# Optimization experiments

Measured on AMD Instinct MI355X. Metric: run time of the kernel, lower is better.

Reference implementation:

```python
import jax, jax.numpy as jnp
import numpy as np

N_NODES = 100000
N_EDGES = 3200000


def _gcn_conv(x, src, dst, W, b, n_nodes):
    # PyG GCNConv: out = D^{-1/2} (A + I) D^{-1/2} X W + b
    h = x @ W  # [N, out]
    # degree of (A + I) counted at targets (symmetric graph assumption as in PyG norm)
    deg = jax.ops.segment_sum(jnp.ones_like(dst, dtype=h.dtype), dst, num_segments=n_nodes)
    dinv = jnp.where(deg > 0, jax.lax.rsqrt(deg), 0.0)
    norm = dinv[src] * dinv[dst]  # [E_total]
    msg = h[src] * norm[:, None]  # gather + normalize  [E_total, out]
    out = jax.ops.segment_sum(msg, dst, num_segments=n_nodes)  # scatter-add
    return out + b


def setup_inputs() -> dict:
    key = jax.random.key(0)
    k1, k2, k3, k4 = jax.random.split(key, 4)
    x = jax.random.normal(k1, (N_NODES, 1), dtype=jnp.float32)
    edge_index = jax.random.randint(k2, (2, N_EDGES), 0, N_NODES, dtype=jnp.int64)
    W1 = jax.random.normal(k3, (1, 64), dtype=jnp.float32) * (1.0 / np.sqrt(1.0))
    b1 = jnp.zeros((64,), dtype=jnp.float32)
    W2 = jax.random.normal(k4, (64, 2), dtype=jnp.float32) * (1.0 / np.sqrt(64.0))
    b2 = jnp.zeros((2,), dtype=jnp.float32)
    return {"x": x, "edge_index": edge_index, "W1": W1, "b1": b1, "W2": W2, "b2": b2}


def reference(x, edge_index, W1, b1, W2, b2):
    n = x.shape[0]
    # add self-loops as GCNConv does by default
    loops = jnp.arange(n, dtype=edge_index.dtype)
    src = jnp.concatenate([edge_index[0], loops])
    dst = jnp.concatenate([edge_index[1], loops])
    h = _gcn_conv(x, src, dst, W1, b1, n)
    h = jax.nn.relu(h)
    h = _gcn_conv(h, src, dst, W2, b2, n)
    h = jax.nn.log_softmax(h, axis=1)
    out = jnp.mean(h, axis=0)
    return out[None, :]  # [1, 2]
```

## Files before the change

### kernel.cpp

```cpp
#include <hip/hip_runtime.h>


#define TPB 512
#define SORT_BLK 256
#define BSHIFT 7
#define BNODES 128
#define MAXBUCK 1024
#define BSTRIDE 6144


__global__ __launch_bounds__(TPB) void k_sort(const int* __restrict__ ei, int E, int epb,
                                              int nbuck, int* __restrict__ gcur,
                                              unsigned* __restrict__ packed) {
    __shared__ int h[MAXBUCK];
    for (int b = threadIdx.x; b < nbuck; b += TPB) h[b] = 0;
    __syncthreads();
    const int4* d4 = (const int4*)(ei + E);
    int nq = epb >> 2;
    int q0 = blockIdx.x * nq;
    for (int j = threadIdx.x; j < nq; j += TPB) {
        int q = q0 + j;
        int e = q << 2;
        if (e + 3 < E) {
            int4 v = d4[q];
            atomicAdd(&h[v.x >> BSHIFT], 1);
            atomicAdd(&h[v.y >> BSHIFT], 1);
            atomicAdd(&h[v.z >> BSHIFT], 1);
            atomicAdd(&h[v.w >> BSHIFT], 1);
        } else {
            for (int k = 0; k < 4; ++k)
                if (e + k < E) atomicAdd(&h[(ei + E)[e + k] >> BSHIFT], 1);
        }
    }
    __syncthreads();
    for (int b = threadIdx.x; b < nbuck; b += TPB) {
        int c = h[b];
        h[b] = c ? atomicAdd(&gcur[b], c) : 0;
    }
    __syncthreads();
    const int4* s4 = (const int4*)ei;
    for (int j = threadIdx.x; j < nq; j += TPB) {
        int q = q0 + j;
        int e = q << 2;
        if (e + 3 < E) {
            int4 vs = s4[q];
            int4 vd = d4[q];
            int b, p;
            b = vd.x >> BSHIFT; p = atomicAdd(&h[b], 1);
            packed[b * BSTRIDE + p] = ((unsigned)(vd.x & (BNODES - 1)) << 17) | (unsigned)vs.x;
            b = vd.y >> BSHIFT; p = atomicAdd(&h[b], 1);
            packed[b * BSTRIDE + p] = ((unsigned)(vd.y & (BNODES - 1)) << 17) | (unsigned)vs.y;
            b = vd.z >> BSHIFT; p = atomicAdd(&h[b], 1);
            packed[b * BSTRIDE + p] = ((unsigned)(vd.z & (BNODES - 1)) << 17) | (unsigned)vs.z;
            b = vd.w >> BSHIFT; p = atomicAdd(&h[b], 1);
            packed[b * BSTRIDE + p] = ((unsigned)(vd.w & (BNODES - 1)) << 17) | (unsigned)vs.w;
        } else {
            for (int k = 0; k < 4; ++k) {
                int ee = e + k;
                if (ee < E) {
                    int s = ei[ee], d = ei[E + ee];
                    int b = d >> BSHIFT;
                    int p = atomicAdd(&h[b], 1);
                    packed[b * BSTRIDE + p] = ((unsigned)(d & (BNODES - 1)) << 17) | (unsigned)s;
                }
            }
        }
    }
}


__global__ __launch_bounds__(TPB) void k_csr(unsigned* __restrict__ packed,
                                             const int* __restrict__ gcur,
                                             const float* __restrict__ x,
                                             float* __restrict__ dinv,
                                             float* __restrict__ u,
                                             int* __restrict__ rptr, int N) {
    __shared__ int cnt[8][BNODES];
    __shared__ int eptr[BNODES];
    __shared__ unsigned stage[BSTRIDE];
    for (int k = threadIdx.x; k < 8 * BNODES; k += TPB) ((int*)cnt)[k] = 0;
    __syncthreads();
    int b = blockIdx.x;
    int sz = gcur[b];
    unsigned* base = packed + (size_t)b * BSTRIDE;
    const uint4* base4 = (const uint4*)base;
    int wv = threadIdx.x >> 6;
    int nq4 = sz >> 2;
    int half = nq4 >> 1;
    for (int j = threadIdx.x; j < half; j += TPB) {
        uint4 p = base4[j];
        uint4 q = base4[j + half];
        atomicAdd(&cnt[wv][(p.x >> 17) & 127], 1);
        atomicAdd(&cnt[wv][(p.y >> 17) & 127], 1);
        atomicAdd(&cnt[wv][(p.z >> 17) & 127], 1);
        atomicAdd(&cnt[wv][(p.w >> 17) & 127], 1);
        atomicAdd(&cnt[wv][(q.x >> 17) & 127], 1);
        atomicAdd(&cnt[wv][(q.y >> 17) & 127], 1);
        atomicAdd(&cnt[wv][(q.z >> 17) & 127], 1);
        atomicAdd(&cnt[wv][(q.w >> 17) & 127], 1);
    }
    for (int j = half * 8 + threadIdx.x; j < sz; j += TPB) {
        unsigned p = base[j];
        atomicAdd(&cnt[wv][(p >> 17) & 127], 1);
    }
    __syncthreads();
    int tot = 0;
    if (threadIdx.x < BNODES) {
        #pragma unroll
        for (int c = 0; c < 8; ++c) tot += cnt[c][threadIdx.x];
        eptr[threadIdx.x] = tot;
    }
    __syncthreads();
    for (int d = 1; d < BNODES; d <<= 1) {
        int add = 0;
        if (threadIdx.x < BNODES && threadIdx.x >= d) add = eptr[threadIdx.x - d];
        __syncthreads();
        if (threadIdx.x < BNODES) eptr[threadIdx.x] += add;
        __syncthreads();
    }
    if (threadIdx.x < BNODES) {
        int t = threadIdx.x;
        int ex = eptr[t] - tot;
        int run = ex;
        #pragma unroll
        for (int c = 0; c < 8; ++c) { int v = cnt[c][t]; cnt[c][t] = run; run += v; }
        rptr[b * BNODES + t] = ex;
        int node = (b << BSHIFT) + t;
        if (node < N) {
            float di = rsqrtf((float)(tot + 1));
            dinv[node] = di;
            u[node] = di * x[node];
        }
    }
    __syncthreads();
    for (int j = threadIdx.x; j < half; j += TPB) {
        uint4 p = base4[j];
        uint4 q = base4[j + half];
        int pos;
        pos = atomicAdd(&cnt[wv][(p.x >> 17) & 127], 1); stage[pos] = p.x & 0x1FFFF;
        pos = atomicAdd(&cnt[wv][(p.y >> 17) & 127], 1); stage[pos] = p.y & 0x1FFFF;
        pos = atomicAdd(&cnt[wv][(p.z >> 17) & 127], 1); stage[pos] = p.z & 0x1FFFF;
        pos = atomicAdd(&cnt[wv][(p.w >> 17) & 127], 1); stage[pos] = p.w & 0x1FFFF;
        pos = atomicAdd(&cnt[wv][(q.x >> 17) & 127], 1); stage[pos] = q.x & 0x1FFFF;
        pos = atomicAdd(&cnt[wv][(q.y >> 17) & 127], 1); stage[pos] = q.y & 0x1FFFF;
        pos = atomicAdd(&cnt[wv][(q.z >> 17) & 127], 1); stage[pos] = q.z & 0x1FFFF;
        pos = atomicAdd(&cnt[wv][(q.w >> 17) & 127], 1); stage[pos] = q.w & 0x1FFFF;
    }
    for (int j = half * 8 + threadIdx.x; j < sz; j += TPB) {
        unsigned p = base[j];
        int pos = atomicAdd(&cnt[wv][(p >> 17) & 127], 1);
        stage[pos] = p & 0x1FFFF;
    }
    __syncthreads();
    for (int k = threadIdx.x; k < sz; k += TPB) base[k] = stage[k];
}


__global__ __launch_bounds__(TPB) void k_agg1(const unsigned* __restrict__ sorted,
                                              const int* __restrict__ gcur,
                                              const int* __restrict__ rptr,
                                              const float* __restrict__ dinv,
                                              const float* __restrict__ u,
                                              const float* __restrict__ W1,
                                              const float* __restrict__ b1,
                                              const float* __restrict__ W2,
                                              float2* __restrict__ w, int N) {
    __shared__ float sW1[64], sb1[64], sW2[128];
    __shared__ int sptr[BNODES + 1];
    int b = blockIdx.x;
    if (threadIdx.x < 64) { sW1[threadIdx.x] = W1[threadIdx.x]; sb1[threadIdx.x] = b1[threadIdx.x]; }
    else if (threadIdx.x < 192) sW2[threadIdx.x - 64] = W2[threadIdx.x - 64];
    if (threadIdx.x < BNODES) sptr[threadIdx.x] = rptr[b * BNODES + threadIdx.x];
    if (threadIdx.x == 0) sptr[BNODES] = gcur[b];
    __syncthreads();
    int t = threadIdx.x >> 2, k = threadIdx.x & 3;
    const unsigned* base = sorted + (size_t)b * BSTRIDE;
    int s0 = sptr[t], s1 = sptr[t + 1];
    float s = 0.f;
    for (int j = s0 + k; j < s1; j += 4) s += u[base[j] & 0x1FFFF];
    s += __shfl_xor(s, 1, 64);
    s += __shfl_xor(s, 2, 64);
    int node = (b << BSHIFT) + t;
    if (k == 0 && node < N) {
        float di = dinv[node];
        float sv = di * (s + u[node]);
        float z0 = 0.f, z1 = 0.f;
        #pragma unroll
        for (int j = 0; j < 64; ++j) {
            float h = fmaxf(fmaf(sv, sW1[j], sb1[j]), 0.f);
            z0 = fmaf(h, sW2[2 * j], z0);
            z1 = fmaf(h, sW2[2 * j + 1], z1);
        }
        w[node] = make_float2(di * z0, di * z1);
    }
}


__global__ __launch_bounds__(TPB) void k_agg2(const unsigned* __restrict__ sorted,
                                              const int* __restrict__ gcur,
                                              const int* __restrict__ rptr,
                                              const float* __restrict__ dinv,
                                              const float2* __restrict__ w,
                                              const float* __restrict__ b2,
                                              float* __restrict__ accum, int N) {
    __shared__ int sptr[BNODES + 1];
    int b = blockIdx.x;
    if (threadIdx.x < BNODES) sptr[threadIdx.x] = rptr[b * BNODES + threadIdx.x];
    if (threadIdx.x == 0) sptr[BNODES] = gcur[b];
    __syncthreads();
    int t = threadIdx.x >> 2, k = threadIdx.x & 3;
    const unsigned* base = sorted + (size_t)b * BSTRIDE;
    int s0 = sptr[t], s1 = sptr[t + 1];
    float sx = 0.f, sy = 0.f;
    for (int j = s0 + k; j < s1; j += 4) {
        float2 v = w[base[j] & 0x1FFFF];
        sx += v.x;
        sy += v.y;
    }
    sx += __shfl_xor(sx, 1, 64); sx += __shfl_xor(sx, 2, 64);
    sy += __shfl_xor(sy, 1, 64); sy += __shfl_xor(sy, 2, 64);
    int node = (b << BSHIFT) + t;
    float l0 = 0.f, l1 = 0.f;
    if (k == 0 && node < N) {
        float di = dinv[node];
        float2 wi = w[node];
        float a0 = di * (sx + wi.x) + b2[0];
        float a1 = di * (sy + wi.y) + b2[1];
        float m = fmaxf(a0, a1);
        float lse = m + logf(expf(a0 - m) + expf(a1 - m));
        l0 = a0 - lse;
        l1 = a1 - lse;
    }
    #pragma unroll
    for (int off = 32; off > 0; off >>= 1) {
        l0 += __shfl_down(l0, off, 64);
        l1 += __shfl_down(l1, off, 64);
    }
    __shared__ float r0[TPB / 64], r1[TPB / 64];
    int wid = threadIdx.x >> 6, lane = threadIdx.x & 63;
    if (lane == 0) { r0[wid] = l0; r1[wid] = l1; }
    __syncthreads();
    if (threadIdx.x == 0) {
        float t0 = 0.f, t1 = 0.f;
        #pragma unroll
        for (int kk = 0; kk < TPB / 64; ++kk) { t0 += r0[kk]; t1 += r1[kk]; }
        accum[2 * b]     = t0;
        accum[2 * b + 1] = t1;
    }
}


#define RTPB 1024
__global__ __launch_bounds__(RTPB) void k_reduce_final(const float* __restrict__ accum,
                                                       int nb, float* __restrict__ out,
                                                       float invN) {
    float t0 = 0.f, t1 = 0.f;
    for (int i = threadIdx.x; i < nb; i += RTPB) {
        t0 += accum[2 * i];
        t1 += accum[2 * i + 1];
    }
    #pragma unroll
    for (int off = 32; off > 0; off >>= 1) {
        t0 += __shfl_down(t0, off, 64);
        t1 += __shfl_down(t1, off, 64);
    }
    __shared__ float s0[RTPB / 64], s1[RTPB / 64];
    int wid = threadIdx.x >> 6, lane = threadIdx.x & 63;
    if (lane == 0) { s0[wid] = t0; s1[wid] = t1; }
    __syncthreads();
    if (threadIdx.x == 0) {
        float a = 0.f, b = 0.f;
        #pragma unroll
        for (int k = 0; k < RTPB / 64; ++k) { a += s0[k]; b += s1[k]; }
        out[0] = a * invN;
        out[1] = b * invN;
    }
}

__global__ void k_finalize(const float* __restrict__ accum, float* __restrict__ out, float invN) {
    out[0] = accum[0] * invN;
    out[1] = accum[1] * invN;
}


#define FTPB 256
__global__ void k_hist(const int* __restrict__ dst, int E, int* __restrict__ deg) {
    int e = blockIdx.x * FTPB + threadIdx.x;
    if (e < E) atomicAdd(&deg[dst[e]], 1);
}
__global__ void k_dinv_u(const int* __restrict__ deg, const float* __restrict__ x,
                         float* __restrict__ dinv, float* __restrict__ u, int N) {
    int i = blockIdx.x * FTPB + threadIdx.x;
    if (i < N) {
        float di = rsqrtf((float)(deg[i] + 1));
        dinv[i] = di;
        u[i] = di * x[i];
    }
}
__global__ void k_scatter1(const int* __restrict__ ei, int E,
                           const float* __restrict__ u, float* __restrict__ t) {
    int e = blockIdx.x * FTPB + threadIdx.x;
    if (e < E) atomicAdd(&t[ei[E + e]], u[ei[e]]);
}
__global__ void k_node_mid_fb(const float* __restrict__ dinv, const float* __restrict__ u,
                              const float* __restrict__ t,
                              const float* __restrict__ W1, const float* __restrict__ b1,
                              const float* __restrict__ W2, float2* __restrict__ w, int N) {
    __shared__ float sW1[64], sb1[64], sW2[128];
    if (threadIdx.x < 64) { sW1[threadIdx.x] = W1[threadIdx.x]; sb1[threadIdx.x] = b1[threadIdx.x]; }
    if (threadIdx.x < 128) sW2[threadIdx.x] = W2[threadIdx.x];
    __syncthreads();
    int i = blockIdx.x * FTPB + threadIdx.x;
    if (i < N) {
        float di = dinv[i];
        float s = di * (t[i] + u[i]);
        float z0 = 0.f, z1 = 0.f;
        #pragma unroll
        for (int j = 0; j < 64; ++j) {
            float h = fmaxf(fmaf(s, sW1[j], sb1[j]), 0.f);
            z0 = fmaf(h, sW2[2 * j], z0);
            z1 = fmaf(h, sW2[2 * j + 1], z1);
        }
        w[i] = make_float2(di * z0, di * z1);
    }
}
__global__ void k_scatter2(const int* __restrict__ ei, int E,
                           const float2* __restrict__ w, float* __restrict__ acc) {
    int e = blockIdx.x * FTPB + threadIdx.x;
    if (e < E) {
        float2 ws = w[ei[e]];
        int d = ei[E + e];
        atomicAdd(&acc[2 * d], ws.x);
        atomicAdd(&acc[2 * d + 1], ws.y);
    }
}
__global__ void k_node_out_fb(const float* __restrict__ dinv, const float2* __restrict__ w,
                              const float2* __restrict__ acc, const float* __restrict__ b2,
                              float* __restrict__ accum, int N) {
    int i = blockIdx.x * FTPB + threadIdx.x;
    float l0 = 0.f, l1 = 0.f;
    if (i < N) {
        float di = dinv[i];
        float2 a = acc[i];
        float2 ww = w[i];
        float a0 = di * (a.x + ww.x) + b2[0];
        float a1 = di * (a.y + ww.y) + b2[1];
        float m = fmaxf(a0, a1);
        float lse = m + logf(expf(a0 - m) + expf(a1 - m));
        l0 = a0 - lse;
        l1 = a1 - lse;
    }
    #pragma unroll
    for (int off = 32; off > 0; off >>= 1) {
        l0 += __shfl_down(l0, off, 64);
        l1 += __shfl_down(l1, off, 64);
    }
    __shared__ float s0[FTPB / 64], s1[FTPB / 64];
    int wid = threadIdx.x >> 6, lane = threadIdx.x & 63;
    if (lane == 0) { s0[wid] = l0; s1[wid] = l1; }
    __syncthreads();
    if (threadIdx.x == 0) {
        float t0 = 0.f, t1 = 0.f;
        #pragma unroll
        for (int k = 0; k < FTPB / 64; ++k) { t0 += s0[k]; t1 += s1[k]; }
        atomicAdd(&accum[0], t0);
        atomicAdd(&accum[1], t1);
    }
}

extern "C" void kernel_launch(void* const* d_in, const int* in_sizes, int n_in,
                              void* d_out, int out_size, void* d_ws, size_t ws_size,
                              hipStream_t stream) {
    const float* x  = (const float*)d_in[0];
    const int*   ei = (const int*)d_in[1];
    const float* W1 = (const float*)d_in[2];
    const float* b1 = (const float*)d_in[3];
    const float* W2 = (const float*)d_in[4];
    const float* b2 = (const float*)d_in[5];
    float* out = (float*)d_out;

    const int N = in_sizes[0];
    const int E = in_sizes[1] / 2;
    const int nbuck = (N + BNODES - 1) >> BSHIFT;
    const int gridN = (N + FTPB - 1) / FTPB;
    const int gridE = (E + FTPB - 1) / FTPB;

    size_t offPacked = 0;
    size_t offW      = offPacked + (size_t)nbuck * BSTRIDE * 4;
    size_t offDinv   = offW + (size_t)N * 8;
    size_t offU      = offDinv + (size_t)N * 4;
    size_t offGcur   = offU + (size_t)N * 4;
    size_t offAccum  = offGcur + (size_t)nbuck * 4;
    size_t offRptr   = offAccum + (size_t)2 * nbuck * 4;
    size_t need      = offRptr + (size_t)nbuck * BNODES * 4;

    if (ws_size >= need && nbuck <= MAXBUCK && N <= (1 << 17)) {
        unsigned* packed = (unsigned*)((char*)d_ws + offPacked);
        float2*   w      = (float2*)((char*)d_ws + offW);
        float*    dinv   = (float*)((char*)d_ws + offDinv);
        float*    u      = (float*)((char*)d_ws + offU);
        int*      gcur   = (int*)((char*)d_ws + offGcur);
        float*    accum  = (float*)((char*)d_ws + offAccum);
        int*      rptr   = (int*)((char*)d_ws + offRptr);

        hipMemsetAsync(gcur, 0, (size_t)nbuck * 4, stream);

        int epb = (((E + SORT_BLK - 1) / SORT_BLK) + 3) & ~3;

        k_sort<<<SORT_BLK, TPB, 0, stream>>>(ei, E, epb, nbuck, gcur, packed);
        k_csr<<<nbuck, TPB, 0, stream>>>(packed, gcur, x, dinv, u, rptr, N);
        k_agg1<<<nbuck, TPB, 0, stream>>>(packed, gcur, rptr, dinv, u, W1, b1, W2, w, N);
        k_agg2<<<nbuck, TPB, 0, stream>>>(packed, gcur, rptr, dinv, (const float2*)w, b2, accum, N);
        k_reduce_final<<<1, RTPB, 0, stream>>>(accum, nbuck, out, 1.0f / (float)N);
    } else {
        int*   deg   = (int*)d_ws;
        float* t     = (float*)(deg + N);
        float* acc   = t + N;
        float* accum = acc + 2 * N;
        float* dinv  = accum + 2;
        float* u     = dinv + N;
        float2* w    = (float2*)(u + N);
        hipMemsetAsync(d_ws, 0, (size_t)(4 * N + 2) * sizeof(float), stream);
        k_hist<<<gridE, FTPB, 0, stream>>>(ei + E, E, deg);
        k_dinv_u<<<gridN, FTPB, 0, stream>>>(deg, x, dinv, u, N);
        k_scatter1<<<gridE, FTPB, 0, stream>>>(ei, E, u, t);
        k_node_mid_fb<<<gridN, FTPB, 0, stream>>>(dinv, u, t, W1, b1, W2, w, N);
        k_scatter2<<<gridE, FTPB, 0, stream>>>(ei, E, w, acc);
        k_node_out_fb<<<gridN, FTPB, 0, stream>>>(dinv, w, (const float2*)acc, b2, accum, N);
        k_finalize<<<1, 64, 0, stream>>>(accum, out, 1.0f / (float)N);
    }
}
```

Baseline: 164.8 us.

## Compute degrees with global atomics during sort and fuse CSR build into aggregation

The bucket sort kernel now also counts per-node in-degree with global atomics. The separate counting pass in the CSR kernel is dropped, and the placement pass moves into the first aggregation kernel. That kernel builds offsets from a prefix scan of the degrees and gathers u directly from the shared-memory staging buffer. A small kernel computes u from the degrees, and dinv and rptr are recomputed from segment lengths instead of stored. This removes one pass over the packed edges and one kernel's shared-memory histogram, at the cost of 3.2M global atomics on a degree array, which may contend.

```diff
diff --git a/kernel.cpp b/kernel.cpp
--- a/kernel.cpp
+++ b/kernel.cpp
@@ -11,7 +11,8 @@
 
 __global__ __launch_bounds__(TPB) void k_sort(const int* __restrict__ ei, int E, int epb,
                                               int nbuck, int* __restrict__ gcur,
-                                              unsigned* __restrict__ packed) {
+                                              unsigned* __restrict__ packed,
+                                              int* __restrict__ deg) {
     __shared__ int h[MAXBUCK];
     for (int b = threadIdx.x; b < nbuck; b += TPB) h[b] = 0;
     __syncthreads();
@@ -27,9 +28,17 @@
             atomicAdd(&h[v.y >> BSHIFT], 1);
             atomicAdd(&h[v.z >> BSHIFT], 1);
             atomicAdd(&h[v.w >> BSHIFT], 1);
+            atomicAdd(&deg[v.x], 1);
+            atomicAdd(&deg[v.y], 1);
+            atomicAdd(&deg[v.z], 1);
+            atomicAdd(&deg[v.w], 1);
         } else {
             for (int k = 0; k < 4; ++k)
-                if (e + k < E) atomicAdd(&h[(ei + E)[e + k] >> BSHIFT], 1);
+                if (e + k < E) {
+                    int d = (ei + E)[e + k];
+                    atomicAdd(&h[d >> BSHIFT], 1);
+                    atomicAdd(&deg[d], 1);
+                }
         }
     }
     __syncthreads();
@@ -69,120 +78,80 @@
 }
 
 
-__global__ __launch_bounds__(TPB) void k_csr(unsigned* __restrict__ packed,
-                                             const int* __restrict__ gcur,
-                                             const float* __restrict__ x,
-                                             float* __restrict__ dinv,
-                                             float* __restrict__ u,
-                                             int* __restrict__ rptr, int N) {
-    __shared__ int cnt[8][BNODES];
-    __shared__ int eptr[BNODES];
+__global__ __launch_bounds__(TPB) void k_u(const int* __restrict__ deg,
+                                           const float* __restrict__ x,
+                                           float* __restrict__ u, int N) {
+    int i = blockIdx.x * TPB + threadIdx.x;
+    if (i < N) u[i] = rsqrtf((float)(deg[i] + 1)) * x[i];
+}
+
+
+__global__ __launch_bounds__(TPB) void k_csr_agg1(unsigned* __restrict__ packed,
+                                                  const int* __restrict__ deg,
+                                                  const float* __restrict__ u,
+                                                  const float* __restrict__ W1,
+                                                  const float* __restrict__ b1,
+                                                  const float* __restrict__ W2,
+                                                  float2* __restrict__ w, int N) {
     __shared__ unsigned stage[BSTRIDE];
-    for (int k = threadIdx.x; k < 8 * BNODES; k += TPB) ((int*)cnt)[k] = 0;
-    __syncthreads();
-    int b = blockIdx.x;
-    int sz = gcur[b];
+    __shared__ int seg[BNODES + 1];
+    __shared__ int cur[BNODES];
+    __shared__ float sW1[64], sb1[64], sW2[128];
+    const int tid = threadIdx.x;
+    const int b = blockIdx.x;
+    if (tid < 64) { sW1[tid] = W1[tid]; sb1[tid] = b1[tid]; }
+    else if (tid < 192) sW2[tid - 64] = W2[tid - 64];
+    int mydeg = 0;
+    if (tid < BNODES) {
+        int node = (b << BSHIFT) + tid;
+        mydeg = (node < N) ? deg[node] : 0;
+        seg[tid] = mydeg;
+    }
+    __syncthreads();
+    for (int d = 1; d < BNODES; d <<= 1) {
+        int add = 0;
+        if (tid < BNODES && tid >= d) add = seg[tid - d];
+        __syncthreads();
+        if (tid < BNODES) seg[tid] += add;
+        __syncthreads();
+    }
+    if (tid == BNODES - 1) seg[BNODES] = seg[tid];
+    if (tid < BNODES) { seg[tid] -= mydeg; cur[tid] = seg[tid]; }
+    __syncthreads();
+    const int sz = seg[BNODES];
     unsigned* base = packed + (size_t)b * BSTRIDE;
     const uint4* base4 = (const uint4*)base;
-    int wv = threadIdx.x >> 6;
     int nq4 = sz >> 2;
     int half = nq4 >> 1;
-    for (int j = threadIdx.x; j < half; j += TPB) {
-        uint4 p = base4[j];
-        uint4 q = base4[j + half];
-        atomicAdd(&cnt[wv][(p.x >> 17) & 127], 1);
-        atomicAdd(&cnt[wv][(p.y >> 17) & 127], 1);
-        atomicAdd(&cnt[wv][(p.z >> 17) & 127], 1);
-        atomicAdd(&cnt[wv][(p.w >> 17) & 127], 1);
-        atomicAdd(&cnt[wv][(q.x >> 17) & 127], 1);
-        atomicAdd(&cnt[wv][(q.y >> 17) & 127], 1);
-        atomicAdd(&cnt[wv][(q.z >> 17) & 127], 1);
-        atomicAdd(&cnt[wv][(q.w >> 17) & 127], 1);
-    }
-    for (int j = half * 8 + threadIdx.x; j < sz; j += TPB) {
-        unsigned p = base[j];
-        atomicAdd(&cnt[wv][(p >> 17) & 127], 1);
-    }
-    __syncthreads();
-    int tot = 0;
-    if (threadIdx.x < BNODES) {
-        #pragma unroll
-        for (int c = 0; c < 8; ++c) tot += cnt[c][threadIdx.x];
-        eptr[threadIdx.x] = tot;
-    }
-    __syncthreads();
-    for (int d = 1; d < BNODES; d <<= 1) {
-        int add = 0;
-        if (threadIdx.x < BNODES && threadIdx.x >= d) add = eptr[threadIdx.x - d];
-        __syncthreads();
-        if (threadIdx.x < BNODES) eptr[threadIdx.x] += add;
-        __syncthreads();
-    }
-    if (threadIdx.x < BNODES) {
-        int t = threadIdx.x;
-        int ex = eptr[t] - tot;
-        int run = ex;
-        #pragma unroll
-        for (int c = 0; c < 8; ++c) { int v = cnt[c][t]; cnt[c][t] = run; run += v; }
-        rptr[b * BNODES + t] = ex;
-        int node = (b << BSHIFT) + t;
-        if (node < N) {
-            float di = rsqrtf((float)(tot + 1));
-            dinv[node] = di;
-            u[node] = di * x[node];
-        }
-    }
-    __syncthreads();
-    for (int j = threadIdx.x; j < half; j += TPB) {
+    for (int j = tid; j < half; j += TPB) {
         uint4 p = base4[j];
         uint4 q = base4[j + half];
         int pos;
-        pos = atomicAdd(&cnt[wv][(p.x >> 17) & 127], 1); stage[pos] = p.x & 0x1FFFF;
-        pos = atomicAdd(&cnt[wv][(p.y >> 17) & 127], 1); stage[pos] = p.y & 0x1FFFF;
-        pos = atomicAdd(&cnt[wv][(p.z >> 17) & 127], 1); stage[pos] = p.z & 0x1FFFF;
-        pos = atomicAdd(&cnt[wv][(p.w >> 17) & 127], 1); stage[pos] = p.w & 0x1FFFF;
-        pos = atomicAdd(&cnt[wv][(q.x >> 17) & 127], 1); stage[pos] = q.x & 0x1FFFF;
-        pos = atomicAdd(&cnt[wv][(q.y >> 17) & 127], 1); stage[pos] = q.y & 0x1FFFF;
-        pos = atomicAdd(&cnt[wv][(q.z >> 17) & 127], 1); stage[pos] = q.z & 0x1FFFF;
-        pos = atomicAdd(&cnt[wv][(q.w >> 17) & 127], 1); stage[pos] = q.w & 0x1FFFF;
-    }
-    for (int j = half * 8 + threadIdx.x; j < sz; j += TPB) {
+        pos = atomicAdd(&cur[(p.x >> 17) & 127], 1); stage[pos] = p.x & 0x1FFFF;
+        pos = atomicAdd(&cur[(p.y >> 17) & 127], 1); stage[pos] = p.y & 0x1FFFF;
+        pos = atomicAdd(&cur[(p.z >> 17) & 127], 1); stage[pos] = p.z & 0x1FFFF;
+        pos = atomicAdd(&cur[(p.w >> 17) & 127], 1); stage[pos] = p.w & 0x1FFFF;
+        pos = atomicAdd(&cur[(q.x >> 17) & 127], 1); stage[pos] = q.x & 0x1FFFF;
+        pos = atomicAdd(&cur[(q.y >> 17) & 127], 1); stage[pos] = q.y & 0x1FFFF;
+        pos = atomicAdd(&cur[(q.z >> 17) & 127], 1); stage[pos] = q.z & 0x1FFFF;
+        pos = atomicAdd(&cur[(q.w >> 17) & 127], 1); stage[pos] = q.w & 0x1FFFF;
+    }
+    for (int j = half * 8 + tid; j < sz; j += TPB) {
         unsigned p = base[j];
-        int pos = atomicAdd(&cnt[wv][(p >> 17) & 127], 1);
+        int pos = atomicAdd(&cur[(p >> 17) & 127], 1);
         stage[pos] = p & 0x1FFFF;
     }
     __syncthreads();
-    for (int k = threadIdx.x; k < sz; k += TPB) base[k] = stage[k];
-}
-
-
-__global__ __launch_bounds__(TPB) void k_agg1(const unsigned* __restrict__ sorted,
-                                              const int* __restrict__ gcur,
-                                              const int* __restrict__ rptr,
-                                              const float* __restrict__ dinv,
-                                              const float* __restrict__ u,
-                                              const float* __restrict__ W1,
-                                              const float* __restrict__ b1,
-                                              const float* __restrict__ W2,
-                                              float2* __restrict__ w, int N) {
-    __shared__ float sW1[64], sb1[64], sW2[128];
-    __shared__ int sptr[BNODES + 1];
-    int b = blockIdx.x;
-    if (threadIdx.x < 64) { sW1[threadIdx.x] = W1[threadIdx.x]; sb1[threadIdx.x] = b1[threadIdx.x]; }
-    else if (threadIdx.x < 192) sW2[threadIdx.x - 64] = W2[threadIdx.x - 64];
-    if (threadIdx.x < BNODES) sptr[threadIdx.x] = rptr[b * BNODES + threadIdx.x];
-    if (threadIdx.x == 0) sptr[BNODES] = gcur[b];
-    __syncthreads();
-    int t = threadIdx.x >> 2, k = threadIdx.x & 3;
-    const unsigned* base = sorted + (size_t)b * BSTRIDE;
-    int s0 = sptr[t], s1 = sptr[t + 1];
+    for (int k = tid; k < sz; k += TPB) base[k] = stage[k];
+    int t = tid >> 2, k4 = tid & 3;
+    int s0 = seg[t], s1 = seg[t + 1];
     float s = 0.f;
-    for (int j = s0 + k; j < s1; j += 4) s += u[base[j] & 0x1FFFF];
+    for (int j = s0 + k4; j < s1; j += 4) s += u[stage[j]];
     s += __shfl_xor(s, 1, 64);
     s += __shfl_xor(s, 2, 64);
     int node = (b << BSHIFT) + t;
-    if (k == 0 && node < N) {
-        float di = dinv[node];
+    if (k4 == 0 && node < N) {
+        float di = rsqrtf((float)((s1 - s0) + 1));
         float sv = di * (s + u[node]);
         float z0 = 0.f, z1 = 0.f;
         #pragma unroll
@@ -197,23 +166,36 @@
 
 
 __global__ __launch_bounds__(TPB) void k_agg2(const unsigned* __restrict__ sorted,
-                                              const int* __restrict__ gcur,
-                                              const int* __restrict__ rptr,
-                                              const float* __restrict__ dinv,
+                                              const int* __restrict__ deg,
                                               const float2* __restrict__ w,
                                               const float* __restrict__ b2,
                                               float* __restrict__ accum, int N) {
-    __shared__ int sptr[BNODES + 1];
-    int b = blockIdx.x;
-    if (threadIdx.x < BNODES) sptr[threadIdx.x] = rptr[b * BNODES + threadIdx.x];
-    if (threadIdx.x == 0) sptr[BNODES] = gcur[b];
-    __syncthreads();
-    int t = threadIdx.x >> 2, k = threadIdx.x & 3;
+    __shared__ int seg[BNODES + 1];
+    const int tid = threadIdx.x;
+    const int b = blockIdx.x;
+    int mydeg = 0;
+    if (tid < BNODES) {
+        int node = (b << BSHIFT) + tid;
+        mydeg = (node < N) ? deg[node] : 0;
+        seg[tid] = mydeg;
+    }
+    __syncthreads();
+    for (int d = 1; d < BNODES; d <<= 1) {
+        int add = 0;
+        if (tid < BNODES && tid >= d) add = seg[tid - d];
+        __syncthreads();
+        if (tid < BNODES) seg[tid] += add;
+        __syncthreads();
+    }
+    if (tid == BNODES - 1) seg[BNODES] = seg[tid];
+    if (tid < BNODES) seg[tid] -= mydeg;
+    __syncthreads();
+    int t = tid >> 2, k4 = tid & 3;
     const unsigned* base = sorted + (size_t)b * BSTRIDE;
-    int s0 = sptr[t], s1 = sptr[t + 1];
+    int s0 = seg[t], s1 = seg[t + 1];
     float sx = 0.f, sy = 0.f;
-    for (int j = s0 + k; j < s1; j += 4) {
-        float2 v = w[base[j] & 0x1FFFF];
+    for (int j = s0 + k4; j < s1; j += 4) {
+        float2 v = w[base[j]];
         sx += v.x;
         sy += v.y;
     }
@@ -221,8 +203,8 @@
     sy += __shfl_xor(sy, 1, 64); sy += __shfl_xor(sy, 2, 64);
     int node = (b << BSHIFT) + t;
     float l0 = 0.f, l1 = 0.f;
-    if (k == 0 && node < N) {
-        float di = dinv[node];
+    if (k4 == 0 && node < N) {
+        float di = rsqrtf((float)((s1 - s0) + 1));
         float2 wi = w[node];
         float a0 = di * (sx + wi.x) + b2[0];
         float a1 = di * (sy + wi.y) + b2[1];
@@ -237,10 +219,10 @@
         l1 += __shfl_down(l1, off, 64);
     }
     __shared__ float r0[TPB / 64], r1[TPB / 64];
-    int wid = threadIdx.x >> 6, lane = threadIdx.x & 63;
+    int wid = tid >> 6, lane = tid & 63;
     if (lane == 0) { r0[wid] = l0; r1[wid] = l1; }
     __syncthreads();
-    if (threadIdx.x == 0) {
+    if (tid == 0) {
         float t0 = 0.f, t1 = 0.f;
         #pragma unroll
         for (int kk = 0; kk < TPB / 64; ++kk) { t0 += r0[kk]; t1 += r1[kk]; }
@@ -387,30 +369,28 @@
 
     size_t offPacked = 0;
     size_t offW      = offPacked + (size_t)nbuck * BSTRIDE * 4;
-    size_t offDinv   = offW + (size_t)N * 8;
-    size_t offU      = offDinv + (size_t)N * 4;
+    size_t offU      = offW + (size_t)N * 8;
     size_t offGcur   = offU + (size_t)N * 4;
-    size_t offAccum  = offGcur + (size_t)nbuck * 4;
-    size_t offRptr   = offAccum + (size_t)2 * nbuck * 4;
-    size_t need      = offRptr + (size_t)nbuck * BNODES * 4;
+    size_t offDeg    = offGcur + (size_t)nbuck * 4;
+    size_t offAccum  = offDeg + (size_t)N * 4;
+    size_t need      = offAccum + (size_t)2 * nbuck * 4;
 
     if (ws_size >= need && nbuck <= MAXBUCK && N <= (1 << 17)) {
         unsigned* packed = (unsigned*)((char*)d_ws + offPacked);
         float2*   w      = (float2*)((char*)d_ws + offW);
-        float*    dinv   = (float*)((char*)d_ws + offDinv);
         float*    u      = (float*)((char*)d_ws + offU);
         int*      gcur   = (int*)((char*)d_ws + offGcur);
+        int*      deg    = (int*)((char*)d_ws + offDeg);
         float*    accum  = (float*)((char*)d_ws + offAccum);
-        int*      rptr   = (int*)((char*)d_ws + offRptr);
-
-        hipMemsetAsync(gcur, 0, (size_t)nbuck * 4, stream);
+
+        hipMemsetAsync(gcur, 0, (size_t)nbuck * 4 + (size_t)N * 4, stream);
 
         int epb = (((E + SORT_BLK - 1) / SORT_BLK) + 3) & ~3;
 
-        k_sort<<<SORT_BLK, TPB, 0, stream>>>(ei, E, epb, nbuck, gcur, packed);
-        k_csr<<<nbuck, TPB, 0, stream>>>(packed, gcur, x, dinv, u, rptr, N);
-        k_agg1<<<nbuck, TPB, 0, stream>>>(packed, gcur, rptr, dinv, u, W1, b1, W2, w, N);
-        k_agg2<<<nbuck, TPB, 0, stream>>>(packed, gcur, rptr, dinv, (const float2*)w, b2, accum, N);
+        k_sort<<<SORT_BLK, TPB, 0, stream>>>(ei, E, epb, nbuck, gcur, packed, deg);
+        k_u<<<(N + TPB - 1) / TPB, TPB, 0, stream>>>(deg, x, u, N);
+        k_csr_agg1<<<nbuck, TPB, 0, stream>>>(packed, deg, u, W1, b1, W2, w, N);
+        k_agg2<<<nbuck, TPB, 0, stream>>>(packed, deg, (const float2*)w, b2, accum, N);
         k_reduce_final<<<1, RTPB, 0, stream>>>(accum, nbuck, out, 1.0f / (float)N);
     } else {
         int*   deg   = (int*)d_ws;
```

Result: slower. 278.6 us (+69.1%).
